# Performance work log

Hardware: AMD Instinct MI355X
Metric: run time of the kernel (lower is better)

The kernel has to match this reference:

```python
import jax, jax.numpy as jnp
import numpy as np

B, N, F, U = 16, 2048, 64, 64

def setup_inputs() -> dict:
    key = jax.random.key(0)
    k1, k2, k3 = jax.random.split(key, 3)
    node_features = jax.random.normal(k1, (B, N, F), dtype=jnp.float32)
    adjacency_matrix = (jax.random.uniform(k2, (B, N, N)) < 0.01).astype(jnp.float32)
    kernel = jax.random.normal(k3, (F, U), dtype=jnp.float32) * (1.0 / np.sqrt(F))
    return {"node_features": node_features, "adjacency_matrix": adjacency_matrix, "kernel": kernel}

def reference(node_features, adjacency_matrix, kernel):
    # A_tilde = A + I  (self-loops)
    n = adjacency_matrix.shape[-1]
    adj = adjacency_matrix + jnp.eye(n, dtype=adjacency_matrix.dtype)
    # symmetric normalization D^-1/2 A_tilde D^-1/2 (diag matmuls == broadcast scaling)
    row_sum = jnp.sum(adj, axis=-1)                      # [B, N]
    d_inv_sqrt = jnp.where(row_sum > 0, row_sum ** -0.5, 0.0)
    norm_adj = d_inv_sqrt[:, :, None] * adj * d_inv_sqrt[:, None, :]
    # feature transform then aggregate, fused with ReLU
    transformed = jnp.einsum('bnf,fu->bnu', node_features, kernel)
    out = jnp.einsum('bnm,bmu->bnu', norm_adj, transformed)
    return jax.nn.relu(out)
```

## Files before the change

kernel.cpp:

```cpp
#include <hip/hip_runtime.h>
#include <hip/hip_bf16.h>


#define NB     16
#define NN     2048
#define NF     64
#define NU     64
#define NROWS  (NB * NN)

typedef float vfloat4 __attribute__((ext_vector_type(4)));

__global__ __launch_bounds__(256) void k1_rowsum_compact(
    const float* __restrict__ A, float* __restrict__ d,
    int* __restrict__ counts, int2* __restrict__ pairs, int cap)
{
    const int row = blockIdx.x;
    const float* Arow = A + (size_t)row * NN;
    __shared__ int   s_cnt;
    __shared__ float s_part[4];
    if (threadIdx.x == 0) s_cnt = 0;
    __syncthreads();

    const int t = threadIdx.x;
    const int lane = t & 63;
    const size_t base = (size_t)row * cap;
    const unsigned long long lmask_lt = (lane == 63) ? 0x7fffffffffffffffull
                                                     : ((1ull << lane) - 1ull);
    float sum = 0.f;
    #pragma unroll
    for (int k = 0; k < 2; ++k) {
        const int i4 = t + k * 256;
        const vfloat4 a = __builtin_nontemporal_load(
            reinterpret_cast<const vfloat4*>(Arow) + i4);
        #pragma unroll
        for (int c = 0; c < 4; ++c) {
            const float vv = a[c];
            sum += vv;
            const unsigned long long m = __ballot(vv != 0.f);
            if (m) {
                int wb = 0;
                if (lane == 0) wb = atomicAdd(&s_cnt, __popcll(m));
                wb = __shfl(wb, 0);
                if (vv != 0.f) {
                    const int slot = wb + __popcll(m & lmask_lt);
                    if (slot < cap) {
                        int2 e; e.x = i4 * 4 + c; e.y = __float_as_int(vv);
                        pairs[base + slot] = e;
                    }
                }
            }
        }
    }
    #pragma unroll
    for (int o = 32; o > 0; o >>= 1) sum += __shfl_down(sum, o);
    const int wid = t >> 6;
    if (lane == 0) s_part[wid] = sum;
    __syncthreads();
    if (t == 0) {
        const float tot = s_part[0] + s_part[1] + s_part[2] + s_part[3] + 1.0f;
        d[row]      = rsqrtf(tot);
        counts[row] = s_cnt;
    }
}

__global__ __launch_bounds__(256) void k2_transform_scale(
    const float* __restrict__ X, const float* __restrict__ W,
    const float* __restrict__ d, float* __restrict__ Tp)
{
    const int t = threadIdx.x;
    const int lane = t & 63;
    float wcol[NF];
    #pragma unroll
    for (int f = 0; f < NF; ++f) wcol[f] = W[f * NU + lane];

    const int wave_gid = (blockIdx.x * 256 + t) >> 6;
    const int n_waves  = (gridDim.x * 256) >> 6;
    for (int row = wave_gid; row < NROWS; row += n_waves) {
        const float xv = X[(size_t)row * NF + lane];
        float acc = 0.f;
        #pragma unroll
        for (int f = 0; f < NF; ++f) acc += __shfl(xv, f) * wcol[f];
        Tp[(size_t)row * NU + lane] = acc * d[row];
    }
}

__global__ __launch_bounds__(256) void k3_aggregate(
    const float* __restrict__ A, const float* __restrict__ Tp,
    const float* __restrict__ d, const int* __restrict__ counts,
    const int2* __restrict__ pairs, float* __restrict__ out, int cap)
{
    const int t = threadIdx.x;
    const int wid = t >> 6, lane = t & 63;
    const int row = blockIdx.x * 4 + wid;
    const int b   = row >> 11;
    const float* Tb = Tp + (((size_t)b) << 11) * NU;

    float acc = Tp[(size_t)row * NU + lane];
    const int cnt = counts[row];
    if (cnt <= cap) {
        const size_t base = (size_t)row * cap;
        const int4* p4 = reinterpret_cast<const int4*>(pairs + base);
        int k = 0;
        for (; k + 4 <= cnt; k += 4) {
            const int4 q0 = p4[k >> 1];
            const int4 q1 = p4[(k >> 1) + 1];
            const float t0 = Tb[((size_t)q0.x << 6) + lane];
            const float t1 = Tb[((size_t)q0.z << 6) + lane];
            const float t2 = Tb[((size_t)q1.x << 6) + lane];
            const float t3 = Tb[((size_t)q1.z << 6) + lane];
            acc += __int_as_float(q0.y) * t0;
            acc += __int_as_float(q0.w) * t1;
            acc += __int_as_float(q1.y) * t2;
            acc += __int_as_float(q1.w) * t3;
        }
        for (; k < cnt; ++k) {
            const int2 e = pairs[base + k];
            acc += __int_as_float(e.y) * Tb[((size_t)e.x << 6) + lane];
        }
    } else {
        const float* Arow = A + (size_t)row * NN;
        for (int j = 0; j < NN; ++j) {
            const float v = Arow[j];
            if (v != 0.f) acc += v * Tb[((size_t)j << 6) + lane];
        }
    }
    const float r = d[row] * acc;
    out[(size_t)row * NU + lane] = r > 0.f ? r : 0.f;
}

extern "C" void kernel_launch(void* const* d_in, const int* in_sizes, int n_in,
                              void* d_out, int out_size, void* d_ws, size_t ws_size,
                              hipStream_t stream)
{
    const float* X = (const float*)d_in[0];
    const float* A = (const float*)d_in[1];
    const float* W = (const float*)d_in[2];
    float* out = (float*)d_out;

    char* ws = (char*)d_ws;
    float* Tp     = (float*)ws;
    float* dvec   = (float*)(ws + (size_t)NROWS * NU * 4);
    int*   counts = (int*)  (ws + (size_t)NROWS * NU * 4 + (size_t)NROWS * 4);
    int2*  pairs  = (int2*) (ws + (size_t)NROWS * NU * 4 + 2ull * NROWS * 4);

    const size_t fixed = (size_t)NROWS * NU * 4 + 2ull * NROWS * 4;
    int cap = 0;
    if (ws_size > fixed) {
        size_t c = (ws_size - fixed) / ((size_t)NROWS * sizeof(int2));
        cap = (int)(c < 128 ? c : 128);
        cap &= ~1;
    }

    k1_rowsum_compact<<<NROWS, 256, 0, stream>>>(A, dvec, counts, pairs, cap);
    k2_transform_scale<<<1024, 256, 0, stream>>>(X, W, dvec, Tp);
    k3_aggregate<<<NROWS / 4, 256, 0, stream>>>(A, Tp, dvec, counts, pairs, out, cap);
}
```

Before: 404.3 us.

## Process one row per wave with XCD-aware batch mapping across all kernels

```diff
diff --git a/kernel.cpp b/kernel.cpp
--- a/kernel.cpp
+++ b/kernel.cpp
@@ -7,59 +7,60 @@
 #define NF     64
 #define NU     64
 #define NROWS  (NB * NN)
+#define NGRP   (NROWS / 4)
 
 typedef float vfloat4 __attribute__((ext_vector_type(4)));
+
+__device__ __forceinline__ int map_row(int g, int wid) {
+    const int x = g & 7, s = g >> 3;
+    const int batch = x + ((s >> 9) << 3);
+    const int grp = s & 511;
+    return (batch << 11) + (grp << 2) + wid;
+}
 
 __global__ __launch_bounds__(256) void k1_rowsum_compact(
     const float* __restrict__ A, float* __restrict__ d,
     int* __restrict__ counts, int2* __restrict__ pairs, int cap)
 {
-    const int row = blockIdx.x;
+    const int t = threadIdx.x, wid = t >> 6, lane = t & 63;
+    const int row = map_row(blockIdx.x, wid);
     const float* Arow = A + (size_t)row * NN;
-    __shared__ int   s_cnt;
-    __shared__ float s_part[4];
-    if (threadIdx.x == 0) s_cnt = 0;
-    __syncthreads();
-
-    const int t = threadIdx.x;
-    const int lane = t & 63;
-    const size_t base = (size_t)row * cap;
     const unsigned long long lmask_lt = (lane == 63) ? 0x7fffffffffffffffull
                                                      : ((1ull << lane) - 1ull);
+    vfloat4 a[8];
+    #pragma unroll
+    for (int c = 0; c < 8; ++c)
+        a[c] = __builtin_nontemporal_load(
+            reinterpret_cast<const vfloat4*>(Arow) + c * 64 + lane);
+
+    const size_t base = (size_t)row * cap;
+    int cnt = 0;
     float sum = 0.f;
     #pragma unroll
-    for (int k = 0; k < 2; ++k) {
-        const int i4 = t + k * 256;
-        const vfloat4 a = __builtin_nontemporal_load(
-            reinterpret_cast<const vfloat4*>(Arow) + i4);
+    for (int c = 0; c < 8; ++c) {
         #pragma unroll
-        for (int c = 0; c < 4; ++c) {
-            const float vv = a[c];
+        for (int e = 0; e < 4; ++e) {
+            const float vv = a[c][e];
             sum += vv;
             const unsigned long long m = __ballot(vv != 0.f);
             if (m) {
-                int wb = 0;
-                if (lane == 0) wb = atomicAdd(&s_cnt, __popcll(m));
-                wb = __shfl(wb, 0);
                 if (vv != 0.f) {
-                    const int slot = wb + __popcll(m & lmask_lt);
+                    const int slot = cnt + __popcll(m & lmask_lt);
                     if (slot < cap) {
-                        int2 e; e.x = i4 * 4 + c; e.y = __float_as_int(vv);
-                        pairs[base + slot] = e;
+                        int2 p; p.x = ((c * 64 + lane) << 2) + e;
+                        p.y = __float_as_int(vv);
+                        pairs[base + slot] = p;
                     }
                 }
+                cnt += __popcll(m);
             }
         }
     }
     #pragma unroll
-    for (int o = 32; o > 0; o >>= 1) sum += __shfl_down(sum, o);
-    const int wid = t >> 6;
-    if (lane == 0) s_part[wid] = sum;
-    __syncthreads();
-    if (t == 0) {
-        const float tot = s_part[0] + s_part[1] + s_part[2] + s_part[3] + 1.0f;
-        d[row]      = rsqrtf(tot);
-        counts[row] = s_cnt;
+    for (int o = 1; o < 64; o <<= 1) sum += __shfl_xor(sum, o);
+    if (lane == 0) {
+        d[row]      = rsqrtf(sum + 1.0f);
+        counts[row] = cnt;
     }
 }
 
@@ -67,21 +68,22 @@
     const float* __restrict__ X, const float* __restrict__ W,
     const float* __restrict__ d, float* __restrict__ Tp)
 {
-    const int t = threadIdx.x;
-    const int lane = t & 63;
-    float wcol[NF];
+    __shared__ float sW[NF * NU];
+    const int t = threadIdx.x, wid = t >> 6, lane = t & 63;
     #pragma unroll
-    for (int f = 0; f < NF; ++f) wcol[f] = W[f * NU + lane];
+    for (int k = 0; k < 4; ++k)
+        reinterpret_cast<float4*>(sW)[t + 256 * k] =
+            reinterpret_cast<const float4*>(W)[t + 256 * k];
+    __syncthreads();
 
-    const int wave_gid = (blockIdx.x * 256 + t) >> 6;
-    const int n_waves  = (gridDim.x * 256) >> 6;
-    for (int row = wave_gid; row < NROWS; row += n_waves) {
-        const float xv = X[(size_t)row * NF + lane];
-        float acc = 0.f;
-        #pragma unroll
-        for (int f = 0; f < NF; ++f) acc += __shfl(xv, f) * wcol[f];
-        Tp[(size_t)row * NU + lane] = acc * d[row];
-    }
+    const int row = map_row(blockIdx.x, wid);
+    const float xv = X[(size_t)row * NF + lane];
+    const float dr = d[row];
+    float acc = 0.f;
+    #pragma unroll
+    for (int f = 0; f < NF; ++f)
+        acc += __shfl(xv, f) * sW[f * NU + lane];
+    Tp[(size_t)row * NU + lane] = acc * dr;
 }
 
 __global__ __launch_bounds__(256) void k3_aggregate(
@@ -89,9 +91,8 @@
     const float* __restrict__ d, const int* __restrict__ counts,
     const int2* __restrict__ pairs, float* __restrict__ out, int cap)
 {
-    const int t = threadIdx.x;
-    const int wid = t >> 6, lane = t & 63;
-    const int row = blockIdx.x * 4 + wid;
+    const int t = threadIdx.x, wid = t >> 6, lane = t & 63;
+    const int row = map_row(blockIdx.x, wid);
     const int b   = row >> 11;
     const float* Tb = Tp + (((size_t)b) << 11) * NU;
 
@@ -151,7 +152,7 @@
         cap &= ~1;
     }
 
-    k1_rowsum_compact<<<NROWS, 256, 0, stream>>>(A, dvec, counts, pairs, cap);
-    k2_transform_scale<<<1024, 256, 0, stream>>>(X, W, dvec, Tp);
-    k3_aggregate<<<NROWS / 4, 256, 0, stream>>>(A, Tp, dvec, counts, pairs, out, cap);
+    k1_rowsum_compact<<<NGRP, 256, 0, stream>>>(A, dvec, counts, pairs, cap);
+    k2_transform_scale<<<NGRP, 256, 0, stream>>>(X, W, dvec, Tp);
+    k3_aggregate<<<NGRP, 256, 0, stream>>>(A, Tp, dvec, counts, pairs, out, cap);
 }
```

Result: no change. 403.2 us (-0.3%).
